# Optimization experiments

Measured on AMD Instinct MI355X. Metric: run time of the kernel, lower is better.

The kernel has to match this reference:

```python
import jax, jax.numpy as jnp
import numpy as np

D_MODEL = 1024
NUM_HEADS = 16
D_K = D_MODEL // NUM_HEADS
B, T = 2, 2048


def setup_inputs() -> dict:
    key = jax.random.key(0)
    ks = jax.random.split(key, 12)
    s = 1.0 / np.sqrt(D_MODEL)
    inp = {
        "query": jax.random.normal(ks[0], (B, T, D_MODEL), jnp.float32),
        "key": jax.random.normal(ks[1], (B, T, D_MODEL), jnp.float32),
        "value": jax.random.normal(ks[2], (B, T, D_MODEL), jnp.float32),
        "key_padding_mask": jax.random.randint(ks[3], (B, T), 0, 2, jnp.int32),
        "attention_mask": jax.random.randint(ks[4], (B, T, T), 0, 2, jnp.int32),
        "Wq": jax.random.normal(ks[5], (D_MODEL, D_MODEL), jnp.float32) * s,
        "bq": jnp.zeros((D_MODEL,), jnp.float32),
        "Wk": jax.random.normal(ks[6], (D_MODEL, D_MODEL), jnp.float32) * s,
        "bk": jnp.zeros((D_MODEL,), jnp.float32),
        "Wv": jax.random.normal(ks[7], (D_MODEL, D_MODEL), jnp.float32) * s,
        "bv": jnp.zeros((D_MODEL,), jnp.float32),
        "Wo": jax.random.normal(ks[8], (D_MODEL, D_MODEL), jnp.float32) * s,
        "bo": jnp.zeros((D_MODEL,), jnp.float32),
    }
    return inp


def reference(query, key, value, key_padding_mask, attention_mask,
              Wq, bq, Wk, bk, Wv, bv, Wo, bo):
    Bsz, Tq, _ = query.shape
    Tk = key.shape[1]
    min_val = jnp.finfo(query.dtype).min

    def proj(x, W, b):  # [B,T,D] -> [B,H,T,d_k]
        y = x @ W.T + b
        return y.reshape(Bsz, -1, NUM_HEADS, D_K).transpose(0, 2, 1, 3)

    q = proj(query, Wq, bq)
    k = proj(key, Wk, bk)
    v = proj(value, Wv, bv)

    # [B,H,Tq,Tk] scores
    scores = jnp.einsum("bhqd,bhkd->bhqk", q, k) / jnp.sqrt(jnp.asarray(D_K, query.dtype))
    scores = jnp.where(attention_mask[:, None, :, :] == 1, min_val, scores)
    scores = jnp.where(key_padding_mask[:, None, None, :] == 1, min_val, scores)

    attn = jax.nn.softmax(scores, axis=-1)
    out = jnp.einsum("bhqk,bhkd->bqhd", attn, v).reshape(Bsz, Tq, D_MODEL)
    return out @ Wo.T + bo
```

## Files before the change

kernel.cpp:

```cpp
#include <hip/hip_runtime.h>


#define T_SEQ 2048
#define NH 16
#define DM 1024
#define DK 64

typedef __attribute__((ext_vector_type(8))) short bf16x8;
typedef __attribute__((ext_vector_type(4))) float f32x4;
typedef __attribute__((ext_vector_type(4))) unsigned short u16x4;
typedef __attribute__((ext_vector_type(4))) unsigned int u32x4;

__device__ __forceinline__ unsigned short f2bf(float x) {
  union { float f; unsigned int u; } v; v.f = x;
  unsigned int r = v.u + 0x7fffu + ((v.u >> 16) & 1u);
  return (unsigned short)(r >> 16);
}
__device__ __forceinline__ float bf2f(unsigned short h) {
  union { unsigned int u; float f; } v; v.u = ((unsigned int)h) << 16;
  return v.f;
}
__device__ __forceinline__ void gload16(const unsigned short* g, unsigned short* l) {
  __builtin_amdgcn_global_load_lds(
      (const __attribute__((address_space(1))) void*)(g),
      (__attribute__((address_space(3))) void*)(l), 16, 0, 0);
}
__device__ __forceinline__ unsigned int cvtpk(float a, float b) {
  unsigned int r;
  asm("v_cvt_pk_bf16_f32 %0, %1, %2" : "=v"(r) : "v"(a), "v"(b));
  return r;
}

__global__ __launch_bounds__(256) void prep_all(
    const float* __restrict__ Wq, const float* __restrict__ Wk,
    const float* __restrict__ Wv, const float* __restrict__ Wo,
    const float* __restrict__ q, const float* __restrict__ k,
    const float* __restrict__ v,
    const int* __restrict__ am, const int* __restrict__ kpm,
    unsigned short* __restrict__ wq, unsigned short* __restrict__ wk,
    unsigned short* __restrict__ wv, unsigned short* __restrict__ woh,
    unsigned short* __restrict__ qb, unsigned short* __restrict__ kb,
    unsigned short* __restrict__ vb,
    unsigned long long* __restrict__ pm) {
  const int id = blockIdx.x;
  if (id < 4096) {
    const int z = id >> 10;
    const int i = (id & 1023) * 256 + threadIdx.x;
    const float* src = (z == 0) ? Wq : (z == 1) ? Wk : (z == 2) ? Wv : Wo;
    unsigned short* dst = (z == 0) ? wq : (z == 1) ? wk : (z == 2) ? wv : woh;
    f32x4 x = ((const f32x4*)src)[i];
    u16x4 h;
#pragma unroll
    for (int j = 0; j < 4; ++j) h[j] = f2bf(x[j]);
    ((u16x4*)dst)[i] = h;
  } else if (id < 16384) {
    const int t = id - 4096;
    const int z = t >> 12;
    const int i = (t & 4095) * 256 + threadIdx.x;
    const float* src = (z == 0) ? q : (z == 1) ? k : v;
    unsigned short* dst = (z == 0) ? qb : (z == 1) ? kb : vb;
    f32x4 x = ((const f32x4*)src)[i];
    u16x4 h;
#pragma unroll
    for (int j = 0; j < 4; ++j) h[j] = f2bf(x[j]);
    ((u16x4*)dst)[i] = h;
  } else {
    const int w = (id - 16384) * 4 + ((int)threadIdx.x >> 6);
    const int lane = threadIdx.x & 63;
    const int kt = w & 31;
    const int qq = (w >> 5) & 2047;
    const int b = w >> 16;
    const int col = kt * 64 + lane;
    int masked = am[((long)(b * T_SEQ + qq)) * T_SEQ + col] | kpm[b * T_SEQ + col];
    unsigned long long bits = __ballot(masked != 0);
    if (lane == 0) pm[((long)(b * T_SEQ + qq)) * 32 + kt] = bits;
  }
}

template <int EPI, int TERMS, int WM, int WN, int BN>
__device__ __forceinline__ void gemm_body(
    const unsigned short* __restrict__ Ahi,
    const unsigned short* __restrict__ Bhi, const unsigned short* __restrict__ Blo,
    const float* __restrict__ bias, unsigned short* __restrict__ Chi,
    float* __restrict__ Cf, unsigned short* __restrict__ Vt, int m0, int n0) {
  constexpr int FM = 128 / (WM * 16);
  constexpr int FN = BN / (WN * 16);
  constexpr int AIT = 2;
  constexpr int BIT = (BN * 4) / 256;
  __shared__ alignas(16) unsigned short sAh[2][128 * 32];
  __shared__ alignas(16) unsigned short sBh[2][BN * 32];
  __shared__ alignas(16) unsigned short sBl[TERMS == 2 ? 2 : 1][TERMS == 2 ? BN * 32 : 8];

  const int tid = threadIdx.x;
  const int lane = tid & 63, wid = tid >> 6;
  const int lr = lane & 15, lg = lane >> 4;
  const int wr = wid / WN, wc = wid % WN;

  f32x4 acc[FM][FN];
#pragma unroll
  for (int i = 0; i < FM; ++i)
#pragma unroll
    for (int j = 0; j < FN; ++j) acc[i][j] = (f32x4){0.f, 0.f, 0.f, 0.f};

  long asrc[AIT], bsrc[BIT];
#pragma unroll
  for (int it = 0; it < AIT; ++it) {
    int c = it * 256 + tid, r = c >> 2;
    int scb = (c & 3) ^ ((r >> 1) & 3);
    asrc[it] = (long)(m0 + r) * DM + scb * 8;
  }
#pragma unroll
  for (int it = 0; it < BIT; ++it) {
    int c = it * 256 + tid, r = c >> 2;
    int scb = (c & 3) ^ ((r >> 1) & 3);
    bsrc[it] = (long)(n0 + r) * DM + scb * 8;
  }

  auto stage = [&](int bi, int kt) {
#pragma unroll
    for (int it = 0; it < AIT; ++it)
      gload16(Ahi + asrc[it] + kt * 32, &sAh[bi][it * 2048 + wid * 512]);
#pragma unroll
    for (int it = 0; it < BIT; ++it) {
      const int dst = it * 2048 + wid * 512;
      gload16(Bhi + bsrc[it] + kt * 32, &sBh[bi][dst]);
      if constexpr (TERMS == 2) gload16(Blo + bsrc[it] + kt * 32, &sBl[bi][dst]);
    }
  };

  stage(0, 0);
  __syncthreads();
  int buf = 0;

  for (int kt = 0; kt < DM / 32; ++kt) {
    if (kt < DM / 32 - 1) stage(buf ^ 1, kt + 1);

    bf16x8 afh[FM], bfh[FN], bfl[FN];
#pragma unroll
    for (int f = 0; f < FM; ++f) {
      int rA = wr * (FM * 16) + f * 16 + lr;
      int iA = rA * 32 + ((lg ^ ((rA >> 1) & 3)) << 3);
      afh[f] = *(const bf16x8*)&sAh[buf][iA];
    }
#pragma unroll
    for (int f = 0; f < FN; ++f) {
      int rB = wc * (FN * 16) + f * 16 + lr;
      int iB = rB * 32 + ((lg ^ ((rB >> 1) & 3)) << 3);
      bfh[f] = *(const bf16x8*)&sBh[buf][iB];
      if constexpr (TERMS == 2) bfl[f] = *(const bf16x8*)&sBl[buf][iB];
    }
#pragma unroll
    for (int fm = 0; fm < FM; ++fm)
#pragma unroll
      for (int fn = 0; fn < FN; ++fn) {
        acc[fm][fn] = __builtin_amdgcn_mfma_f32_16x16x32_bf16(afh[fm], bfh[fn], acc[fm][fn], 0, 0, 0);
        if constexpr (TERMS == 2)
          acc[fm][fn] = __builtin_amdgcn_mfma_f32_16x16x32_bf16(afh[fm], bfl[fn], acc[fm][fn], 0, 0, 0);
      }
    __syncthreads();
    buf ^= 1;
  }

#pragma unroll
  for (int fm = 0; fm < FM; ++fm)
#pragma unroll
    for (int fn = 0; fn < FN; ++fn) {
      const int mb = m0 + wr * (FM * 16) + fm * 16 + lg * 4;
      const int n = n0 + wc * (FN * 16) + fn * 16 + lr;
      float y[4];
#pragma unroll
      for (int i = 0; i < 4; ++i) y[i] = acc[fm][fn][i] + bias[n];
      if constexpr (EPI == 0) {
        if (Vt) {
          int b = mb >> 11, t0 = mb & 2047, hh_ = n >> 6, d = n & 63;
          uint2 w = make_uint2(cvtpk(y[0], y[1]), cvtpk(y[2], y[3]));
          *(uint2*)(Vt + ((long)((b * NH + hh_) * DK + d)) * T_SEQ + t0) = w;
        } else {
#pragma unroll
          for (int i = 0; i < 4; ++i) {
            int m = mb + i;
            int b = m >> 11, t = m & 2047, hh_ = n >> 6, d = n & 63;
            Chi[((long)((b * NH + hh_) * T_SEQ + t)) * DK + d] = f2bf(y[i]);
          }
        }
      } else {
#pragma unroll
        for (int i = 0; i < 4; ++i) Cf[(long)(mb + i) * DM + n] = y[i];
      }
    }
}

__global__ __launch_bounds__(256) void gemm_qkv(
    const unsigned short* __restrict__ Aq, const unsigned short* __restrict__ Ak,
    const unsigned short* __restrict__ Av,
    const unsigned short* __restrict__ Bq, const unsigned short* __restrict__ Bk,
    const unsigned short* __restrict__ Bv,
    const float* __restrict__ bq, const float* __restrict__ bk, const float* __restrict__ bv,
    unsigned short* __restrict__ Qh, unsigned short* __restrict__ Kh,
    unsigned short* __restrict__ Vt) {
  int id = (blockIdx.z * 32 + blockIdx.y) * 8 + blockIdx.x;
  int wg = (id & 7) * 96 + (id >> 3);
  int bx = wg & 7, by = (wg >> 3) & 31, bz = wg >> 8;
  const unsigned short* A = (bz == 0) ? Aq : (bz == 1) ? Ak : Av;
  const unsigned short* Bh = (bz == 0) ? Bq : (bz == 1) ? Bk : Bv;
  const float* bias = (bz == 0) ? bq : (bz == 1) ? bk : bv;
  gemm_body<0, 1, 2, 2, 128>(A, Bh, nullptr, bias,
                             (bz == 0) ? Qh : (bz == 1) ? Kh : nullptr,
                             nullptr, (bz == 2) ? Vt : nullptr,
                             by * 128, bx * 128);
}

__global__ __launch_bounds__(256) void gemm_out(
    const unsigned short* __restrict__ Ah,
    const unsigned short* __restrict__ Bh,
    const float* __restrict__ bias, float* __restrict__ Cf) {
  int id = blockIdx.y * 16 + blockIdx.x;
  int wg = (id & 7) * 64 + (id >> 3);
  int bx = wg & 15, by = wg >> 4;
  gemm_body<1, 1, 4, 1, 64>(Ah, Bh, nullptr, bias, nullptr, Cf, nullptr,
                            by * 128, bx * 64);
}

__global__ __launch_bounds__(512) void attn_fwd(
    const unsigned short* __restrict__ qhi, const unsigned short* __restrict__ khi,
    const unsigned short* __restrict__ vthi,
    const unsigned long long* __restrict__ pm,
    unsigned short* __restrict__ ohi) {
  __shared__ alignas(16) unsigned short sK[2][64 * 64];
  __shared__ alignas(16) unsigned short sV[2][64 * 64];

  const int tid = threadIdx.x;
  const int lane = tid & 63, wid = tid >> 6;
  const int lr = lane & 15, lg = lane >> 4;
  int id = blockIdx.y * 16 + blockIdx.x;
  int wg = (id & 7) * 64 + (id >> 3);
  const int qblk = wg & 15, bh = wg >> 4;
  const int b = bh >> 4, h = bh & 15;
  const int qw = qblk * 128 + wid * 16;

  const int r0 = wid * 8 + (lane >> 3);
  const int scb = (lane & 7) ^ (r0 & 7);
  auto perm = [](int r) {
    int tn = r >> 4, g = (r >> 2) & 3, i = r & 3;
    return (tn >> 1) * 32 + g * 8 + (tn & 1) * 4 + i;
  };
  const unsigned short* kS = khi + ((long)bh * T_SEQ + perm(r0)) * DK + scb * 8;
  const unsigned short* vS = vthi + ((long)bh * DK + r0) * T_SEQ + scb * 8;

  const float C = 0.125f * 1.44269504f;
  bf16x8 aqh[2];
  {
    const unsigned short* qp = qhi + ((long)bh * T_SEQ + qw + lr) * DK + lg * 8;
    aqh[0] = *(const bf16x8*)qp;
    aqh[1] = *(const bf16x8*)(qp + 32);
#pragma unroll
    for (int ks = 0; ks < 2; ++ks)
#pragma unroll
      for (int j = 0; j < 8; ++j)
        aqh[ks][j] = (short)f2bf(bf2f((unsigned short)aqh[ks][j]) * C);
  }
  bf16x8 vone;
#pragma unroll
  for (int j = 0; j < 8; ++j) vone[j] = (short)0x3F80;

  const unsigned long long* pmrow = pm + ((long)b * T_SEQ + qw + lr) * 32;
  f32x4 accO[4];
  f32x4 accL = (f32x4){0.f, 0.f, 0.f, 0.f};
#pragma unroll
  for (int i = 0; i < 4; ++i) accO[i] = (f32x4){0.f, 0.f, 0.f, 0.f};

  auto stage = [&](int bi, int kb) {
    gload16(kS + (long)kb * DK, &sK[bi][wid * 512]);
    gload16(vS + kb, &sV[bi][wid * 512]);
  };

  stage(0, 0);
  __syncthreads();
  int buf = 0;
  unsigned long long pmv = pmrow[0];

  for (int kt = 0; kt < T_SEQ / 64; ++kt) {
    if (kt < T_SEQ / 64 - 1) stage(buf ^ 1, (kt + 1) * 64);
    unsigned long long pmn = pmrow[(kt + 1) & 31];

    f32x4 s[4];
    __builtin_amdgcn_s_setprio(1);
#pragma unroll
    for (int tn = 0; tn < 4; ++tn) {
      f32x4 a = (f32x4){-12.f, -12.f, -12.f, -12.f};
#pragma unroll
      for (int ks = 0; ks < 2; ++ks) {
        int r = tn * 16 + lr;
        int idx = r * 64 + (((ks * 4 + lg) ^ (r & 7)) << 3);
        bf16x8 khf = *(const bf16x8*)&sK[buf][idx];
        a = __builtin_amdgcn_mfma_f32_16x16x32_bf16(khf, aqh[ks], a, 0, 0, 0);
      }
      s[tn] = a;
    }
    __builtin_amdgcn_s_setprio(0);

    unsigned int mlo = (unsigned int)(pmv >> (lg * 8));
    unsigned int mhi = (unsigned int)(pmv >> (lg * 8 + 32));
    float p[4][4];
#pragma unroll
    for (int tn = 0; tn < 4; ++tn) {
      unsigned int mm = (tn & 2) ? mhi : mlo;
#pragma unroll
      for (int i = 0; i < 4; ++i) {
        float sv = ((mm >> ((tn & 1) * 4 + i)) & 1u) ? -1e30f : s[tn][i];
        p[tn][i] = __builtin_amdgcn_exp2f(sv);
      }
    }
    bf16x8 bp[2];
#pragma unroll
    for (int ks2 = 0; ks2 < 2; ++ks2) {
      u32x4 t;
      t[0] = cvtpk(p[2 * ks2][0], p[2 * ks2][1]);
      t[1] = cvtpk(p[2 * ks2][2], p[2 * ks2][3]);
      t[2] = cvtpk(p[2 * ks2 + 1][0], p[2 * ks2 + 1][1]);
      t[3] = cvtpk(p[2 * ks2 + 1][2], p[2 * ks2 + 1][3]);
      bp[ks2] = *(bf16x8*)&t;
    }

    __builtin_amdgcn_s_setprio(1);
#pragma unroll
    for (int ks2 = 0; ks2 < 2; ++ks2) {
      accL = __builtin_amdgcn_mfma_f32_16x16x32_bf16(vone, bp[ks2], accL, 0, 0, 0);
#pragma unroll
      for (int dn = 0; dn < 4; ++dn) {
        int rr = dn * 16 + lr;
        int idx = rr * 64 + (((ks2 * 4 + lg) ^ (rr & 7)) << 3);
        bf16x8 vh = *(const bf16x8*)&sV[buf][idx];
        accO[dn] = __builtin_amdgcn_mfma_f32_16x16x32_bf16(vh, bp[ks2], accO[dn], 0, 0, 0);
      }
    }
    __builtin_amdgcn_s_setprio(0);
    __syncthreads();
    buf ^= 1;
    pmv = pmn;
  }

  {
    float inv = 1.0f / fmaxf(accL[0], 1e-30f);
    int q = qw + lr;
    long obase = ((long)(b * T_SEQ + q)) * DM + h * DK;
#pragma unroll
    for (int dn = 0; dn < 4; ++dn) {
      f32x4 vv = accO[dn];
      vv *= inv;
      uint2 w = make_uint2(cvtpk(vv[0], vv[1]), cvtpk(vv[2], vv[3]));
      *(uint2*)(ohi + obase + dn * 16 + lg * 4) = w;
    }
  }
}

extern "C" void kernel_launch(void* const* d_in, const int* in_sizes, int n_in,
                              void* d_out, int out_size, void* d_ws, size_t ws_size,
                              hipStream_t stream) {
  const float* query = (const float*)d_in[0];
  const float* key_i = (const float*)d_in[1];
  const float* value = (const float*)d_in[2];
  const int* kpm = (const int*)d_in[3];
  const int* am = (const int*)d_in[4];
  const float* Wq = (const float*)d_in[5];
  const float* bq = (const float*)d_in[6];
  const float* Wk = (const float*)d_in[7];
  const float* bk = (const float*)d_in[8];
  const float* Wv = (const float*)d_in[9];
  const float* bv = (const float*)d_in[10];
  const float* Wo = (const float*)d_in[11];
  const float* bo = (const float*)d_in[12];
  float* out = (float*)d_out;

  const size_t MB = 1024ull * 1024ull;
  char* ws = (char*)d_ws;
  if (ws_size < 60 * MB) return;

  unsigned short* qbf = (unsigned short*)(ws + 0 * MB);
  unsigned short* kbf = (unsigned short*)(ws + 8 * MB);
  unsigned short* vbf = (unsigned short*)(ws + 16 * MB);
  unsigned short* q_hi = (unsigned short*)(ws + 24 * MB);
  unsigned short* k_hi = (unsigned short*)(ws + 32 * MB);
  unsigned short* vt_hi = (unsigned short*)(ws + 40 * MB);
  unsigned short* wq_hi = (unsigned short*)(ws + 48 * MB);
  unsigned short* wk_hi = (unsigned short*)(ws + 50 * MB);
  unsigned short* wv_hi = (unsigned short*)(ws + 52 * MB);
  unsigned short* wo_hi = (unsigned short*)(ws + 54 * MB);
  unsigned long long* pmask = (unsigned long long*)(ws + 58 * MB);
  unsigned short* o_hi = qbf;

  dim3 blk(256);
  prep_all<<<dim3(49152), blk, 0, stream>>>(
      Wq, Wk, Wv, Wo, query, key_i, value, am, kpm,
      wq_hi, wk_hi, wv_hi, wo_hi, qbf, kbf, vbf, pmask);

  gemm_qkv<<<dim3(8, 32, 3), blk, 0, stream>>>(
      qbf, kbf, vbf, wq_hi, wk_hi, wv_hi, bq, bk, bv, q_hi, k_hi, vt_hi);

  attn_fwd<<<dim3(16, 32), dim3(512), 0, stream>>>(q_hi, k_hi, vt_hi, pmask, o_hi);

  gemm_out<<<dim3(16, 32), blk, 0, stream>>>(o_hi, wo_hi, bo, out);
}
```

Baseline: 144.2 us.

## Split attention key range across two blocks and add a reduction kernel

```diff
diff --git a/kernel.cpp b/kernel.cpp
--- a/kernel.cpp
+++ b/kernel.cpp
@@ -225,7 +225,8 @@
     const unsigned short* __restrict__ qhi, const unsigned short* __restrict__ khi,
     const unsigned short* __restrict__ vthi,
     const unsigned long long* __restrict__ pm,
-    unsigned short* __restrict__ ohi) {
+    float* __restrict__ po0, float* __restrict__ po1,
+    float* __restrict__ pl) {
   __shared__ alignas(16) unsigned short sK[2][64 * 64];
   __shared__ alignas(16) unsigned short sV[2][64 * 64];
 
@@ -237,6 +238,8 @@
   const int qblk = wg & 15, bh = wg >> 4;
   const int b = bh >> 4, h = bh & 15;
   const int qw = qblk * 128 + wid * 16;
+  const int zz = blockIdx.z;
+  const int kt0 = zz * 16;
 
   const int r0 = wid * 8 + (lane >> 3);
   const int scb = (lane & 7) ^ (r0 & 7);
@@ -274,14 +277,14 @@
     gload16(vS + kb, &sV[bi][wid * 512]);
   };
 
-  stage(0, 0);
+  stage(0, kt0 * 64);
   __syncthreads();
   int buf = 0;
-  unsigned long long pmv = pmrow[0];
-
-  for (int kt = 0; kt < T_SEQ / 64; ++kt) {
-    if (kt < T_SEQ / 64 - 1) stage(buf ^ 1, (kt + 1) * 64);
-    unsigned long long pmn = pmrow[(kt + 1) & 31];
+  unsigned long long pmv = pmrow[kt0];
+
+  for (int kt = 0; kt < 16; ++kt) {
+    if (kt < 15) stage(buf ^ 1, (kt0 + kt + 1) * 64);
+    unsigned long long pmn = pmrow[kt0 + ((kt + 1) & 15)];
 
     f32x4 s[4];
     __builtin_amdgcn_s_setprio(1);
@@ -341,17 +344,33 @@
   }
 
   {
-    float inv = 1.0f / fmaxf(accL[0], 1e-30f);
     int q = qw + lr;
-    long obase = ((long)(b * T_SEQ + q)) * DM + h * DK;
-#pragma unroll
-    for (int dn = 0; dn < 4; ++dn) {
-      f32x4 vv = accO[dn];
-      vv *= inv;
-      uint2 w = make_uint2(cvtpk(vv[0], vv[1]), cvtpk(vv[2], vv[3]));
-      *(uint2*)(ohi + obase + dn * 16 + lg * 4) = w;
-    }
-  }
+    float* pob = (zz ? po1 : po0) + ((long)(b * T_SEQ + q)) * DM + h * DK;
+#pragma unroll
+    for (int dn = 0; dn < 4; ++dn)
+      *(f32x4*)(pob + dn * 16 + lg * 4) = accO[dn];
+    if (lg == 0) pl[((long)(zz * 32 + bh)) * T_SEQ + q] = accL[0];
+  }
+}
+
+__global__ __launch_bounds__(256) void reduce_o(
+    const float* __restrict__ po0, const float* __restrict__ po1,
+    const float* __restrict__ pl, unsigned short* __restrict__ ohi) {
+  const long e = ((long)blockIdx.x * 256 + threadIdx.x) * 4;
+  const int b = (int)(e >> 21);
+  const int rem = (int)(e & ((1 << 21) - 1));
+  const int q = rem >> 10;
+  const int h = (rem & 1023) >> 6;
+  const int bh = b * NH + h;
+  const float l0 = pl[(long)bh * T_SEQ + q];
+  const float l1 = pl[(long)(32 + bh) * T_SEQ + q];
+  const float inv = 1.0f / fmaxf(l0 + l1, 1e-30f);
+  f32x4 a = *(const f32x4*)(po0 + e);
+  f32x4 c = *(const f32x4*)(po1 + e);
+#pragma unroll
+  for (int j = 0; j < 4; ++j) a[j] = (a[j] + c[j]) * inv;
+  uint2 w = make_uint2(cvtpk(a[0], a[1]), cvtpk(a[2], a[3]));
+  *(uint2*)(ohi + e) = w;
 }
 
 extern "C" void kernel_launch(void* const* d_in, const int* in_sizes, int n_in,
@@ -374,7 +393,7 @@
 
   const size_t MB = 1024ull * 1024ull;
   char* ws = (char*)d_ws;
-  if (ws_size < 60 * MB) return;
+  if (ws_size < 77 * MB) return;
 
   unsigned short* qbf = (unsigned short*)(ws + 0 * MB);
   unsigned short* kbf = (unsigned short*)(ws + 8 * MB);
@@ -387,7 +406,10 @@
   unsigned short* wv_hi = (unsigned short*)(ws + 52 * MB);
   unsigned short* wo_hi = (unsigned short*)(ws + 54 * MB);
   unsigned long long* pmask = (unsigned long long*)(ws + 58 * MB);
-  unsigned short* o_hi = qbf;
+  float* po0 = (float*)(ws + 0 * MB);
+  float* pl = (float*)(ws + 16 * MB);
+  unsigned short* o_hi = (unsigned short*)(ws + 24 * MB);
+  float* po1 = (float*)(ws + 60 * MB);
 
   dim3 blk(256);
   prep_all<<<dim3(49152), blk, 0, stream>>>(
@@ -397,7 +419,10 @@
   gemm_qkv<<<dim3(8, 32, 3), blk, 0, stream>>>(
       qbf, kbf, vbf, wq_hi, wk_hi, wv_hi, bq, bk, bv, q_hi, k_hi, vt_hi);
 
-  attn_fwd<<<dim3(16, 32), dim3(512), 0, stream>>>(q_hi, k_hi, vt_hi, pmask, o_hi);
+  attn_fwd<<<dim3(16, 32, 2), dim3(512), 0, stream>>>(
+      q_hi, k_hi, vt_hi, pmask, po0, po1, pl);
+
+  reduce_o<<<dim3(4096), blk, 0, stream>>>(po0, po1, pl, o_hi);
 
   gemm_out<<<dim3(16, 32), blk, 0, stream>>>(o_hi, wo_hi, bo, out);
 }
```

After: 157.0 us. 8.9% more time.
